# Optimization experiments

Measured on AMD Instinct MI355X. Metric: run time of the kernel, lower is better.

## Reference

```python
import jax, jax.numpy as jnp
import numpy as np
import math

D_MODEL = 2048
NUM_HEADS = 16
D_HEAD = D_MODEL // NUM_HEADS
ROPE_BASE = 10000.0

def _rope(t, pos):
    # t: [b, h, T, d_head]; standard rotate-half RoPE with base 10000.
    T, d = t.shape[-2], t.shape[-1]
    start = max(pos, 0)  # pos < 0 means training / position 0
    inv_freq = 1.0 / (ROPE_BASE ** (jnp.arange(0, d, 2, dtype=jnp.float32) / d))  # [d/2]
    positions = jnp.arange(start, start + T, dtype=jnp.float32)                   # [T]
    ang = positions[:, None] * inv_freq[None, :]                                  # [T, d/2]
    cos, sin = jnp.cos(ang), jnp.sin(ang)
    x1, x2 = t[..., : d // 2], t[..., d // 2 :]
    return jnp.concatenate([x1 * cos - x2 * sin, x1 * sin + x2 * cos], axis=-1)

def setup_inputs() -> dict:
    key = jax.random.key(0)
    kx, kq, kk, kv, kw = jax.random.split(key, 5)
    s = 1.0 / math.sqrt(D_MODEL)
    return {
        "x": jax.random.normal(kx, (2, 2048, D_MODEL), dtype=jnp.float32),
        "q_out": jax.random.normal(kq, (D_MODEL, D_MODEL), dtype=jnp.float32) * s,
        "k_out": jax.random.normal(kk, (D_MODEL, D_MODEL), dtype=jnp.float32) * s,
        "v_out": jax.random.normal(kv, (D_MODEL, D_MODEL), dtype=jnp.float32) * s,
        "w_out": jax.random.normal(kw, (D_MODEL, D_MODEL), dtype=jnp.float32) * s,
        "pos": 0,
    }

def reference(x, q_out, k_out, v_out, w_out, pos):
    b, t, d = x.shape
    h, dh = NUM_HEADS, D_HEAD

    def heads(y):  # [b, t, d] -> [b, h, t, dh]
        return y.reshape(b, t, h, dh).transpose(0, 2, 1, 3)

    q = _rope(heads(jnp.einsum('btd,de->bte', x, q_out)), pos)
    k = _rope(heads(jnp.einsum('btd,de->bte', x, k_out)), pos)
    v = heads(jnp.einsum('btd,de->bte', x, v_out))

    score = jnp.einsum('bhqd,bhkd->bhqk', q, k) / math.sqrt(dh)
    causal = jnp.triu(jnp.ones((t, t), dtype=bool), k=1)  # True above diagonal -> masked
    score = jnp.where(causal, -jnp.inf, score)
    weights = jax.nn.softmax(score, axis=-1)
    ctx = jnp.einsum('bhqk,bhkd->bhqd', weights, v)        # [b, h, t, dh]
    ctx = ctx.transpose(0, 2, 1, 3).reshape(b, t, d)
    return jnp.einsum('btd,de->bte', ctx, w_out)
```

## Files before the change

### kernel.cpp

```cpp
#include <hip/hip_runtime.h>
#include <hip/hip_bf16.h>
#include <math.h>

#define NH 16
#define DH 128
#define DM 2048
#define BB 2
#define TT 2048

typedef unsigned short u16;
typedef __attribute__((ext_vector_type(8))) __bf16 bf16x8;
typedef __attribute__((ext_vector_type(8))) u16 u16x8;
typedef __attribute__((ext_vector_type(4))) u16 u16x4;
typedef __attribute__((ext_vector_type(4))) float f32x4;

__device__ __forceinline__ float bf2f(u16 a){
  union { unsigned u; float f; } v; v.u = ((unsigned)a) << 16; return v.f;
}
__device__ __forceinline__ u16 f2bf(float f){
  union { float f; unsigned u; } v; v.f = f;
  unsigned r = v.u + 0x7fffu + ((v.u >> 16) & 1u);
  return (u16)(r >> 16);
}
__device__ __forceinline__ __bf16 f2bfh(float f){
  u16 r = f2bf(f); __bf16 h; __builtin_memcpy(&h, &r, 2); return h;
}
__device__ __forceinline__ float bfh2f(__bf16 h){
  u16 r; __builtin_memcpy(&r, &h, 2); return bf2f(r);
}

typedef const __attribute__((address_space(1))) unsigned int* gas_p;
typedef __attribute__((address_space(3))) unsigned int* las_p;
__device__ __forceinline__ void gl_lds16(const u16* g, u16* lds_uniform_base){
  __builtin_amdgcn_global_load_lds((gas_p)(const void*)g,
                                   (las_p)(void*)lds_uniform_base, 16, 0, 0);
}

#define SB() do{ asm volatile("" ::: "memory"); \
                 __builtin_amdgcn_s_barrier();  \
                 asm volatile("" ::: "memory"); }while(0)
#define WAITV8 asm volatile("s_waitcnt vmcnt(8)" ::: "memory")
#define WAITV0 asm volatile("s_waitcnt vmcnt(0)" ::: "memory")

__global__ __launch_bounds__(256)
void prep4(const float* __restrict__ w0, const float* __restrict__ w1,
           const float* __restrict__ w2, const float* __restrict__ x,
           u16* __restrict__ dst, u16* __restrict__ xb){
  __shared__ u16 tile[32][33];
  const int z = blockIdx.z;
  const int tx = threadIdx.x, ty = threadIdx.y;
  if (z == 3){
    const int bid = blockIdx.y * 64 + blockIdx.x;
    const int tid = ty * 32 + tx;
    #pragma unroll
    for (int rep = 0; rep < 2; rep++){
      const int i = bid * 512 + rep * 256 + tid;
      const f32x4 v = *(const f32x4*)(x + (size_t)i * 4);
      u16x4 o;
      #pragma unroll
      for (int j = 0; j < 4; j++) o[j] = f2bf(v[j]);
      *(u16x4*)(xb + (size_t)i * 4) = o;
    }
    return;
  }
  const float* W = (z == 0) ? w0 : (z == 1) ? w1 : w2;
  u16* Wt = dst + (size_t)z * DM * DM;
  const int bx = blockIdx.x * 32, by = blockIdx.y * 32;
  #pragma unroll
  for (int i = 0; i < 32; i += 8)
    tile[ty + i][tx] = f2bf(W[(size_t)(by + ty + i) * DM + bx + tx]);
  __syncthreads();
  #pragma unroll
  for (int i = 0; i < 32; i += 8)
    Wt[(size_t)(bx + ty + i) * DM + by + tx] = tile[tx][ty + i];
}

__global__ __launch_bounds__(256)
void transpose2048(const float* __restrict__ W, u16* __restrict__ Wt){
  __shared__ u16 tile[32][33];
  const int tx = threadIdx.x, ty = threadIdx.y;
  const int bx = blockIdx.x * 32, by = blockIdx.y * 32;
  #pragma unroll
  for (int i = 0; i < 32; i += 8)
    tile[ty + i][tx] = f2bf(W[(size_t)(by + ty + i) * DM + bx + tx]);
  __syncthreads();
  #pragma unroll
  for (int i = 0; i < 32; i += 8)
    Wt[(size_t)(bx + ty + i) * DM + by + tx] = tile[tx][ty + i];
}

__global__ __launch_bounds__(256)
void cvt_f32_bf16(const float* __restrict__ src, u16* __restrict__ dst, int n4){
  const int i = blockIdx.x * 256 + threadIdx.x;
  if (i >= n4) return;
  const f32x4 v = *(const f32x4*)(src + (size_t)i * 4);
  u16x4 o;
  #pragma unroll
  for (int j = 0; j < 4; j++) o[j] = f2bf(v[j]);
  *(u16x4*)(dst + (size_t)i * 4) = o;
}

__global__ __launch_bounds__(256)
void gemm_bt(const u16* __restrict__ A, const u16* __restrict__ Bt_base,
             void* __restrict__ C0, u16* __restrict__ Ck, u16* __restrict__ Cv,
             int mode0){
  __shared__ u16 As[2][128][32];
  __shared__ u16 Bs[2][128][32];
  const int z = blockIdx.z;
  const u16* Bt = Bt_base + (size_t)z * DM * DM;
  void* C = (z == 0) ? C0 : (z == 1) ? (void*)Ck : (void*)Cv;
  const int mode = (z == 0) ? mode0 : (z == 1) ? 3 : 2;

  const int tid = threadIdx.x;
  const int wave = tid >> 6, lane = tid & 63;
  const int wm = wave & 1, wn = wave >> 1;
  const int row16 = lane & 15, quad = lane >> 4;
  const int m0 = blockIdx.x * 128, n0 = blockIdx.y * 128;

  const f32x4 zero = {0.f, 0.f, 0.f, 0.f};
  f32x4 acc[4][4];
  #pragma unroll
  for (int i = 0; i < 4; i++)
    #pragma unroll
    for (int j = 0; j < 4; j++) acc[i][j] = zero;

  const int srow = lane >> 2;
  const int scol = (lane & 3) * 8;

  for (int k0 = 0; k0 < DM; k0 += 64){
    #pragma unroll
    for (int c = 0; c < 2; c++){
      const int rbase = wave * 32 + c * 16;
      const u16* pa = A  + (size_t)(m0 + rbase + srow) * DM + k0 + scol;
      const u16* pb = Bt + (size_t)(n0 + rbase + srow) * DM + k0 + scol;
      gl_lds16(pa,      &As[0][rbase][0]);
      gl_lds16(pa + 32, &As[1][rbase][0]);
      gl_lds16(pb,      &Bs[0][rbase][0]);
      gl_lds16(pb + 32, &Bs[1][rbase][0]);
    }
    __syncthreads();
    #pragma unroll
    for (int buf = 0; buf < 2; buf++){
      bf16x8 af[4], bfr[4];
      #pragma unroll
      for (int mt = 0; mt < 4; mt++)
        af[mt] = *(const bf16x8*)&As[buf][wm * 64 + mt * 16 + row16][quad * 8];
      #pragma unroll
      for (int nt = 0; nt < 4; nt++)
        bfr[nt] = *(const bf16x8*)&Bs[buf][wn * 64 + nt * 16 + row16][quad * 8];
      #pragma unroll
      for (int mt = 0; mt < 4; mt++)
        #pragma unroll
        for (int nt = 0; nt < 4; nt++)
          acc[mt][nt] = __builtin_amdgcn_mfma_f32_16x16x32_bf16(af[mt], bfr[nt], acc[mt][nt], 0, 0, 0);
    }
    __syncthreads();
  }

  #pragma unroll
  for (int mt = 0; mt < 4; mt++){
    #pragma unroll
    for (int nt = 0; nt < 4; nt++){
      #pragma unroll
      for (int r = 0; r < 4; r++){
        const int m = m0 + wm * 64 + mt * 16 + quad * 4 + r;
        const int n = n0 + wn * 64 + nt * 16 + row16;
        const int b = m >> 11, t = m & (TT - 1);
        const int hh = n >> 7, dh = n & (DH - 1);
        if (mode == 1){
          ((u16*)C)[(((size_t)(b * NH + hh) * TT + t) * DH) + dh] = f2bf(acc[mt][nt][r]);
        } else if (mode == 3){
          const int dhs = dh ^ ((t & 7) << 3);
          ((u16*)C)[(((size_t)(b * NH + hh) * TT + t) * DH) + dhs] = f2bf(acc[mt][nt][r]);
        } else if (mode == 2){
          const int ts = (t & 63) ^ ((dh & 7) << 3);
          ((u16*)C)[(((size_t)(b * NH + hh) * 32 + (t >> 6)) * 8192) + dh * 64 + ts] = f2bf(acc[mt][nt][r]);
        } else {
          ((float*)C)[(size_t)m * DM + n] = acc[mt][nt][r];
        }
      }
    }
  }
}

__global__ __launch_bounds__(256)
void ropek(u16* __restrict__ kb, const int* __restrict__ posp){
  const int idx = blockIdx.x * 256 + threadIdx.x;
  const int sub = idx & 7;
  const int row = idx >> 3;
  const int t = row & (TT - 1);
  int p0 = *posp; if (p0 < 0) p0 = 0;
  const float tf = (float)(p0 + t);
  const size_t base = (size_t)row * DH + sub * 8;
  u16x8 lo = *(const u16x8*)(kb + base);
  u16x8 hi = *(const u16x8*)(kb + base + 64);
  const int fx = (t & 7) << 3;
  #pragma unroll
  for (int j = 0; j < 8; j++){
    const int pl = (sub * 8 + j) ^ fx;
    const float inv = __expf(-(float)pl * (9.2103403719761836f / 64.f));
    const float a = tf * inv;
    const float sn = __sinf(a), cs = __cosf(a);
    const float k1 = bf2f(lo[j]), k2 = bf2f(hi[j]);
    lo[j] = f2bf(k1 * cs - k2 * sn);
    hi[j] = f2bf(k1 * sn + k2 * cs);
  }
  *(u16x8*)(kb + base)      = lo;
  *(u16x8*)(kb + base + 64) = hi;
}

template<bool MASK>
__device__ __forceinline__ void attn_tile(
    int kt0, int qbase, int wave, int row16, int quad,
    const bf16x8 (&qf)[4],
    u16 (&k_s)[64][128], u16 (&vt_s)[128][64], u16 (&p_s)[4][16][68],
    f32x4 (&o_acc)[8], float (&l_acc)[4])
{
  const float scale = 0.08838834764831845f;
  const f32x4 zero = {0.f, 0.f, 0.f, 0.f};
  const int fx = (row16 & 7) << 3;
  f32x4 s_acc[4];
  #pragma unroll
  for (int nt = 0; nt < 4; nt++) s_acc[nt] = zero;
  __builtin_amdgcn_s_setprio(1);
  #pragma unroll
  for (int st = 0; st < 4; st++)
    #pragma unroll
    for (int nt = 0; nt < 4; nt++){
      const bf16x8 kf = *(const bf16x8*)&k_s[nt * 16 + row16][(st * 32 + quad * 8) ^ fx];
      s_acc[nt] = __builtin_amdgcn_mfma_f32_16x16x32_bf16(qf[st], kf, s_acc[nt], 0, 0, 0);
    }
  __builtin_amdgcn_s_setprio(0);
  #pragma unroll
  for (int r = 0; r < 4; r++){
    float ps = 0.f;
    #pragma unroll
    for (int nt = 0; nt < 4; nt++){
      float p = __expf(s_acc[nt][r] * scale);
      if (MASK){
        const int qr = qbase + quad * 4 + r;
        if (kt0 + nt * 16 + row16 > qr) p = 0.f;
      }
      ps += p;
      p_s[wave][quad * 4 + r][nt * 16 + row16] = f2bf(p);
    }
    l_acc[r] += ps;
  }
  asm volatile("" ::: "memory");

  __builtin_amdgcn_s_setprio(1);
  #pragma unroll
  for (int kk = 0; kk < 2; kk++){
    const bf16x8 pf = *(const bf16x8*)&p_s[wave][row16][kk * 32 + quad * 8];
    #pragma unroll
    for (int nd = 0; nd < 8; nd++){
      const bf16x8 vb = *(const bf16x8*)&vt_s[nd * 16 + row16][(kk * 32 + quad * 8) ^ fx];
      o_acc[nd] = __builtin_amdgcn_mfma_f32_16x16x32_bf16(pf, vb, o_acc[nd], 0, 0, 0);
    }
  }
  __builtin_amdgcn_s_setprio(0);
}

__device__ __forceinline__ void qload_rope(
    const u16* __restrict__ q, size_t bho, int qbase, int p0,
    int row16, int quad, bf16x8 (&qf)[4])
{
  const u16* qp = q + bho + (size_t)(qbase + row16) * DH + quad * 8;
  #pragma unroll
  for (int st = 0; st < 4; st++) qf[st] = *(const bf16x8*)(qp + st * 32);
  const float tf = (float)(p0 + qbase + row16);
  #pragma unroll
  for (int st = 0; st < 2; st++){
    #pragma unroll
    for (int j = 0; j < 8; j++){
      const int dh = st * 32 + quad * 8 + j;
      const float inv = __expf(-(float)dh * (9.2103403719761836f / 64.f));
      const float a = tf * inv;
      const float sn = __sinf(a), cs = __cosf(a);
      const float lo = bfh2f(qf[st][j]), hi = bfh2f(qf[st + 2][j]);
      qf[st][j]     = f2bfh(lo * cs - hi * sn);
      qf[st + 2][j] = f2bfh(lo * sn + hi * cs);
    }
  }
}

__device__ __forceinline__ void owrite(
    u16* __restrict__ ctx, int bh, int qbase, int row16, int quad,
    f32x4 (&o_acc)[8], float (&l_acc)[4])
{
  #pragma unroll
  for (int r = 0; r < 4; r++){
    #pragma unroll
    for (int off = 1; off < 16; off <<= 1) l_acc[r] += __shfl_xor(l_acc[r], off, 64);
  }
  const int b = bh >> 4, h = bh & 15;
  #pragma unroll
  for (int nd = 0; nd < 8; nd++){
    #pragma unroll
    for (int r = 0; r < 4; r++){
      const int qr = qbase + quad * 4 + r;
      const size_t off = ((size_t)b * TT + qr) * DM + h * DH + nd * 16 + row16;
      ctx[off] = f2bf(o_acc[nd][r] / l_acc[r]);
    }
  }
}

__global__ __launch_bounds__(256)
void attn_fwd(const u16* __restrict__ q, const u16* __restrict__ k,
              const u16* __restrict__ vtg, u16* __restrict__ ctx,
              const int* __restrict__ posp){
  __shared__ u16 k_s[2][64][128];
  __shared__ u16 vt_s[2][128][64];
  __shared__ u16 p_s[4][16][68];
  const int tid = threadIdx.x;
  const int wave = tid >> 6, lane = tid & 63;
  const int row16 = lane & 15, quad = lane >> 4;
  const int i = blockIdx.x;
  const int bh = blockIdx.y;
  int p0 = *posp; if (p0 < 0) p0 = 0;
  const size_t bho = (size_t)bh * TT * DH;

  const int qbH = (31 - i) * 64 + wave * 16;
  const int qbL = i * 64 + wave * 16;
  const int nT = 32 - i;

  bf16x8 qfH[4], qfL[4];
  qload_rope(q, bho, qbH, p0, row16, quad, qfH);
  qload_rope(q, bho, qbL, p0, row16, quad, qfL);

  float lH[4] = {0.f, 0.f, 0.f, 0.f}, lL[4] = {0.f, 0.f, 0.f, 0.f};
  const f32x4 zero = {0.f, 0.f, 0.f, 0.f};
  f32x4 oH[8], oL[8];
  #pragma unroll
  for (int j = 0; j < 8; j++){ oH[j] = zero; oL[j] = zero; }

  const int kl_r = lane >> 4, kl_c = (lane & 15) * 8;
  const int vl_r = lane >> 3, vl_c = (lane & 7) * 8;

  #define ASTAGE(t, db) do{ \
    const int kt = (t) * 64; \
    _Pragma("unroll") \
    for (int u = 0; u < 4; u++){ \
      const int rb = wave * 16 + u * 4; \
      gl_lds16(k + bho + (size_t)(kt + rb + kl_r) * DH + kl_c, &k_s[db][rb][0]); \
    } \
    const u16* vpan = vtg + ((size_t)bh * 32 + (t)) * 8192; \
    _Pragma("unroll") \
    for (int u = 0; u < 4; u++){ \
      const int rb = wave * 32 + u * 8; \
      gl_lds16(vpan + (size_t)(rb + vl_r) * 64 + vl_c, &vt_s[db][rb][0]); \
    } \
  }while(0)

  ASTAGE(0, 0);
  for (int t = 0; t < nT; ++t){
    const int db = t & 1;
    if (t + 1 < nT){
      ASTAGE(t + 1, db ^ 1);
      WAITV8;
    } else {
      WAITV0;
    }
    SB();
    if (t < nT - 1)
      attn_tile<false>(t * 64, qbH, wave, row16, quad, qfH, k_s[db], vt_s[db], p_s, oH, lH);
    else
      attn_tile<true >(t * 64, qbH, wave, row16, quad, qfH, k_s[db], vt_s[db], p_s, oH, lH);
    if (t < i)
      attn_tile<false>(t * 64, qbL, wave, row16, quad, qfL, k_s[db], vt_s[db], p_s, oL, lL);
    else if (t == i)
      attn_tile<true >(t * 64, qbL, wave, row16, quad, qfL, k_s[db], vt_s[db], p_s, oL, lL);
    SB();
  }
  #undef ASTAGE

  owrite(ctx, bh, qbH, row16, quad, oH, lH);
  owrite(ctx, bh, qbL, row16, quad, oL, lL);
}

extern "C" void kernel_launch(void* const* d_in, const int* in_sizes, int n_in,
                              void* d_out, int out_size, void* d_ws, size_t ws_size,
                              hipStream_t stream){
  const float* x  = (const float*)d_in[0];
  const float* wq = (const float*)d_in[1];
  const float* wk = (const float*)d_in[2];
  const float* wv = (const float*)d_in[3];
  const float* wo = (const float*)d_in[4];
  const int* pos  = (const int*)d_in[5];

  char* ws = (char*)d_ws;
  const dim3 tg(64, 64), tb(32, 8);

  if (ws_size >= 92274688ull){
    u16* xb  = (u16*)ws;                  u16* cb = xb;
    u16* wt3 = (u16*)(ws + 16777216);
    u16* qb  = (u16*)(ws + 41943040);
    u16* kb  = (u16*)(ws + 58720256);
    u16* vtg = (u16*)(ws + 75497472);

    prep4<<<dim3(64, 64, 4), tb, 0, stream>>>(wq, wk, wv, x, wt3, xb);
    gemm_bt<<<dim3(32, 16, 3), 256, 0, stream>>>(xb, wt3, qb, kb, vtg, 1);
    transpose2048<<<tg, tb, 0, stream>>>(wo, wt3);
    ropek<<<2048, 256, 0, stream>>>(kb, pos);
    attn_fwd<<<dim3(16, 32), 256, 0, stream>>>(qb, kb, vtg, cb, pos);
    gemm_bt<<<dim3(32, 16, 1), 256, 0, stream>>>(cb, wt3, d_out, 0, 0, 0);
  } else {
    u16* xb  = (u16*)ws;                  u16* cb = xb;
    u16* wt  = (u16*)(ws + 16777216);
    u16* qb  = (u16*)(ws + 25165824);
    u16* kb  = (u16*)(ws + 41943040);
    u16* vtg = (u16*)(ws + 58720256);

    cvt_f32_bf16<<<8192, 256, 0, stream>>>(x, xb, 2097152);
    transpose2048<<<tg, tb, 0, stream>>>(wq, wt);
    gemm_bt<<<dim3(32, 16, 1), 256, 0, stream>>>(xb, wt, qb, 0, 0, 1);
    transpose2048<<<tg, tb, 0, stream>>>(wk, wt);
    gemm_bt<<<dim3(32, 16, 1), 256, 0, stream>>>(xb, wt, kb, 0, 0, 3);
    transpose2048<<<tg, tb, 0, stream>>>(wv, wt);
    gemm_bt<<<dim3(32, 16, 1), 256, 0, stream>>>(xb, wt, vtg, 0, 0, 2);
    ropek<<<2048, 256, 0, stream>>>(kb, pos);
    attn_fwd<<<dim3(16, 32), 256, 0, stream>>>(qb, kb, vtg, cb, pos);
    transpose2048<<<tg, tb, 0, stream>>>(wo, wt);
    gemm_bt<<<dim3(32, 16, 1), 256, 0, stream>>>(cb, wt, d_out, 0, 0, 0);
  }
}
```

Measured before the change: 405.7 us.

## Add 8-wave 128x256 tile GEMM kernel for projections

```diff
diff --git a/kernel.cpp b/kernel.cpp
--- a/kernel.cpp
+++ b/kernel.cpp
@@ -183,6 +183,97 @@
   }
 }
 
+__global__ __launch_bounds__(512)
+void gemm8w(const u16* __restrict__ A, const u16* __restrict__ Bt_base,
+            void* __restrict__ C0, u16* __restrict__ Ck, u16* __restrict__ Cv,
+            int mode0){
+  __shared__ u16 As[2][128][64];
+  __shared__ u16 Bs[2][256][64];
+  const int z = blockIdx.z;
+  const u16* Bt = Bt_base + (size_t)z * DM * DM;
+  void* C = (z == 0) ? C0 : (z == 1) ? (void*)Ck : (void*)Cv;
+  const int mode = (z == 0) ? mode0 : (z == 1) ? 3 : 2;
+
+  const int tid = threadIdx.x;
+  const int wave = tid >> 6, lane = tid & 63;
+  const int wm = wave >> 2, wn = wave & 3;
+  const int row16 = lane & 15, quad = lane >> 4;
+  const int m0 = blockIdx.x * 128, n0 = blockIdx.y * 256;
+
+  const f32x4 zero = {0.f, 0.f, 0.f, 0.f};
+  f32x4 acc[4][4];
+  #pragma unroll
+  for (int i = 0; i < 4; i++)
+    #pragma unroll
+    for (int j = 0; j < 4; j++) acc[i][j] = zero;
+
+  const int sr = lane >> 3;
+  const int sc = ((lane & 7) ^ sr) * 8;
+  const u16* aB = A  + (size_t)(m0 + wave * 16 + sr) * DM + sc;
+  const u16* bB = Bt + (size_t)(n0 + wave * 32 + sr) * DM + sc;
+
+  #define STG8(bf, ku) do{ \
+    gl_lds16(aB + (ku),                     &As[bf][wave * 16][0]); \
+    gl_lds16(aB + (ku) + (size_t)8 * DM,    &As[bf][wave * 16 + 8][0]); \
+    _Pragma("unroll") \
+    for (int u = 0; u < 4; u++) \
+      gl_lds16(bB + (ku) + (size_t)(u * 8) * DM, &Bs[bf][wave * 32 + u * 8][0]); \
+  }while(0)
+
+  STG8(0, 0);
+  __syncthreads();
+
+  for (int t = 0; t < 32; ++t){
+    const int buf = t & 1;
+    if (t < 31) STG8(buf ^ 1, (t + 1) * 64);
+    #pragma unroll
+    for (int kk = 0; kk < 2; kk++){
+      const int pc = ((kk * 4 + quad) ^ (row16 & 7)) * 8;
+      bf16x8 af[4], bk[4];
+      #pragma unroll
+      for (int mt = 0; mt < 4; mt++)
+        af[mt] = *(const bf16x8*)&As[buf][wm * 64 + mt * 16 + row16][pc];
+      #pragma unroll
+      for (int nt = 0; nt < 4; nt++)
+        bk[nt] = *(const bf16x8*)&Bs[buf][wn * 64 + nt * 16 + row16][pc];
+      __builtin_amdgcn_s_setprio(1);
+      #pragma unroll
+      for (int mt = 0; mt < 4; mt++)
+        #pragma unroll
+        for (int nt = 0; nt < 4; nt++)
+          acc[mt][nt] = __builtin_amdgcn_mfma_f32_16x16x32_bf16(af[mt], bk[nt], acc[mt][nt], 0, 0, 0);
+      __builtin_amdgcn_s_setprio(0);
+    }
+    __syncthreads();
+  }
+  #undef STG8
+
+  #pragma unroll
+  for (int mt = 0; mt < 4; mt++){
+    #pragma unroll
+    for (int nt = 0; nt < 4; nt++){
+      #pragma unroll
+      for (int r = 0; r < 4; r++){
+        const int m = m0 + wm * 64 + mt * 16 + quad * 4 + r;
+        const int n = n0 + wn * 64 + nt * 16 + row16;
+        const int b = m >> 11, t = m & (TT - 1);
+        const int hh = n >> 7, dh = n & (DH - 1);
+        if (mode == 1){
+          ((u16*)C)[(((size_t)(b * NH + hh) * TT + t) * DH) + dh] = f2bf(acc[mt][nt][r]);
+        } else if (mode == 3){
+          const int dhs = dh ^ ((t & 7) << 3);
+          ((u16*)C)[(((size_t)(b * NH + hh) * TT + t) * DH) + dhs] = f2bf(acc[mt][nt][r]);
+        } else if (mode == 2){
+          const int ts = (t & 63) ^ ((dh & 7) << 3);
+          ((u16*)C)[(((size_t)(b * NH + hh) * 32 + (t >> 6)) * 8192) + dh * 64 + ts] = f2bf(acc[mt][nt][r]);
+        } else {
+          ((float*)C)[(size_t)m * DM + n] = acc[mt][nt][r];
+        }
+      }
+    }
+  }
+}
+
 __global__ __launch_bounds__(256)
 void ropek(u16* __restrict__ kb, const int* __restrict__ posp){
   const int idx = blockIdx.x * 256 + threadIdx.x;
@@ -399,11 +490,11 @@
     u16* vtg = (u16*)(ws + 75497472);
 
     prep4<<<dim3(64, 64, 4), tb, 0, stream>>>(wq, wk, wv, x, wt3, xb);
-    gemm_bt<<<dim3(32, 16, 3), 256, 0, stream>>>(xb, wt3, qb, kb, vtg, 1);
+    gemm8w<<<dim3(32, 8, 3), 512, 0, stream>>>(xb, wt3, qb, kb, vtg, 1);
     transpose2048<<<tg, tb, 0, stream>>>(wo, wt3);
     ropek<<<2048, 256, 0, stream>>>(kb, pos);
     attn_fwd<<<dim3(16, 32), 256, 0, stream>>>(qb, kb, vtg, cb, pos);
-    gemm_bt<<<dim3(32, 16, 1), 256, 0, stream>>>(cb, wt3, d_out, 0, 0, 0);
+    gemm8w<<<dim3(32, 8, 1), 512, 0, stream>>>(cb, wt3, d_out, 0, 0, 0);
   } else {
     u16* xb  = (u16*)ws;                  u16* cb = xb;
     u16* wt  = (u16*)(ws + 16777216);
```

After: 422.4 us. +4.1%, slower.
